# Performance work log

Measured on AMD Instinct MI355X. Metric: run time of the kernel, lower is better.

Reference implementation:

```python
import jax, jax.numpy as jnp
import numpy as np

# dims: N batch, L seq, H heads, d projection_dim, P position_dimension
N, Lq, Lk, H, d, P = 2, 1024, 1024, 8, 64, 1
D = H * d


def _kernel(x):
    # _log_exp_kernel: positive feature map log(1+exp(x)) (softplus)
    return jax.nn.softplus(x)


def setup_inputs() -> dict:
    key = jax.random.key(0)
    ks = jax.random.split(key, 8)
    sc = 1.0 / np.sqrt(D).astype(np.float32)
    return {
        "query": jax.random.normal(ks[0], (N, Lq, D), jnp.float32),
        "key_seq": jax.random.normal(ks[1], (N, Lk, D), jnp.float32),
        "Wq": jax.random.normal(ks[2], (D, D), jnp.float32) * sc,
        "Wk": jax.random.normal(ks[3], (D, D), jnp.float32) * sc,
        "Wv": jax.random.normal(ks[4], (D, D), jnp.float32) * sc,
        "position_coeffs": jax.random.uniform(ks[5], (H, d), jnp.float32, 0.5, 1.5),
        "position_weight": jax.random.normal(ks[6], (H, d, P), jnp.float32) * 1e-3,
        "position_bias": jax.random.normal(ks[7], (H, d), jnp.float32) * 1e-2,
    }


def reference(query, key_seq, Wq, Wk, Wv, position_coeffs, position_weight, position_bias):
    # torch Linear (no bias): y = x @ W.T
    q = _kernel(jnp.einsum('nld,ed->nle', query, Wq).reshape(N, Lq, H, d))
    k = _kernel(jnp.einsum('nld,ed->nle', key_seq, Wk).reshape(N, Lk, H, d))
    v = jnp.einsum('nld,ed->nle', key_seq, Wv).reshape(N, Lk, H, d)
    # (N, H, L, d)
    q = jnp.transpose(q, (0, 2, 1, 3))
    k = jnp.transpose(k, (0, 2, 1, 3))
    v = jnp.transpose(v, (0, 2, 1, 3))

    # default positions: arange, query_offset = 0
    qpos = jnp.broadcast_to(jnp.arange(Lq, dtype=jnp.float32).reshape(1, Lq, 1), (N, Lq, P))
    kpos = jnp.broadcast_to(jnp.arange(Lk, dtype=jnp.float32).reshape(1, Lk, 1), (N, Lk, P))
    pq = jnp.einsum('nlp,hkp->nhlk', qpos, position_weight) + position_bias[None, :, None, :]
    pk = jnp.einsum('nlp,hkp->nhlk', kpos, position_weight)

    coeff = position_coeffs[None, :, None, :]  # (1, H, 1, d)

    def part(f, values):
        # causal (mask_future) linear attention via inclusive cumsum over keys
        Qf = q * f(pq) * coeff           # (N, H, Lq, d)
        Kf = k * f(pk)                   # (N, H, Lk, d)
        S = jnp.cumsum(jnp.einsum('nhkd,nhke->nhkde', Kf, values), axis=2)
        return jnp.einsum('nhqd,nhqde->nhqe', Qf, S)

    num = part(jnp.cos, v) + part(jnp.sin, v)           # (N, H, Lq, d)
    unit = jnp.ones((N, H, Lk, 1), jnp.float32)
    den = part(jnp.cos, unit) + part(jnp.sin, unit)     # (N, H, Lq, 1)
    attn = num / den
    return jnp.transpose(attn, (0, 2, 1, 3)).reshape(N, Lq, D)
```

## Files before the change

### kernel.cpp

```cpp
#include <hip/hip_runtime.h>
#include <cmath>

#define NB    2
#define LSEQ  1024
#define NH    8
#define HD    64
#define DD    512
#define FDIM  128
#define EV    65
#define SEP   80
#define CHUNK 64
#define NC    16
#define NBH   16

typedef short short8 __attribute__((ext_vector_type(8)));
typedef float floatx4 __attribute__((ext_vector_type(4)));

__device__ __forceinline__ float softplusf(float x) {
  return fmaxf(x, 0.0f) + log1pf(expf(-fabsf(x)));
}

__device__ __forceinline__ unsigned short f2bf(float f) {
  unsigned u = __float_as_uint(f);
  u += 0x7fffu + ((u >> 16) & 1u);
  return (unsigned short)(u >> 16);
}

__device__ __forceinline__ short8 cvt8(float4 a, float4 b) {
  short8 r;
  r[0] = (short)f2bf(a.x); r[1] = (short)f2bf(a.y);
  r[2] = (short)f2bf(a.z); r[3] = (short)f2bf(a.w);
  r[4] = (short)f2bf(b.x); r[5] = (short)f2bf(b.y);
  r[6] = (short)f2bf(b.z); r[7] = (short)f2bf(b.w);
  return r;
}

__global__ __launch_bounds__(256) void k_proj(
    const float* __restrict__ Xq, const float* __restrict__ Xkv,
    const float* __restrict__ Wq, const float* __restrict__ Wk,
    const float* __restrict__ Wv, const float* __restrict__ pw,
    const float* __restrict__ pb, const float* __restrict__ pc,
    float* __restrict__ Qf, float* __restrict__ Kf, float* __restrict__ Vx)
{
  __shared__ short Al[64][72];
  __shared__ short Bl[64][72];
  const int b = blockIdx.x;
  int m0, e0, pmode;
  const float *X, *W;
  if (b < 256) {
    m0 = (b >> 3) << 6; e0 = (b & 7) << 6;
    X = Xq; W = Wq + (size_t)e0 * DD; pmode = 0;
  } else {
    const int bb = b - 256;
    m0 = (bb >> 4) << 6;
    const int nt = bb & 15;
    e0 = (nt & 7) << 6;
    X = Xkv;
    if (nt < 8) { W = Wk + (size_t)e0 * DD; pmode = 1; }
    else        { W = Wv + (size_t)e0 * DD; pmode = 2; }
  }
  const int tid  = threadIdx.x;
  const int r    = tid >> 2;
  const int ko   = (tid & 3) << 4;
  const int wave = tid >> 6, lane = tid & 63;
  const int quad = lane >> 4, lm = lane & 15;
  const float* Ag = X + (size_t)(m0 + r) * DD + ko;
  const float* Bg = W + (size_t)r * DD + ko;
  float4 a[4], bb4[4];
#pragma unroll
  for (int u = 0; u < 4; ++u) {
    a[u]   = *(const float4*)(Ag + (u << 2));
    bb4[u] = *(const float4*)(Bg + (u << 2));
  }
  floatx4 acc[4] = {};
  for (int k0 = 0; k0 < DD; k0 += 64) {
    __syncthreads();
    *(short8*)&Al[r][ko]     = cvt8(a[0], a[1]);
    *(short8*)&Al[r][ko + 8] = cvt8(a[2], a[3]);
    *(short8*)&Bl[r][ko]     = cvt8(bb4[0], bb4[1]);
    *(short8*)&Bl[r][ko + 8] = cvt8(bb4[2], bb4[3]);
    __syncthreads();
    if (k0 + 64 < DD) {
#pragma unroll
      for (int u = 0; u < 4; ++u) {
        a[u]   = *(const float4*)(Ag + k0 + 64 + (u << 2));
        bb4[u] = *(const float4*)(Bg + k0 + 64 + (u << 2));
      }
    }
#pragma unroll
    for (int ks = 0; ks < 2; ++ks) {
      const short8 af = *(const short8*)&Al[(wave << 4) + lm][(quad << 3) + (ks << 5)];
#pragma unroll
      for (int t = 0; t < 4; ++t) {
        const short8 bf = *(const short8*)&Bl[(t << 4) + lm][(quad << 3) + (ks << 5)];
        acc[t] = __builtin_amdgcn_mfma_f32_16x16x32_bf16(af, bf, acc[t], 0, 0, 0);
      }
    }
  }
#pragma unroll
  for (int t = 0; t < 4; ++t) {
    const int e = e0 + (t << 4) + lm;
    const int h = e >> 6, jj = e & 63;
    if (pmode == 2) {
#pragma unroll
      for (int rg = 0; rg < 4; ++rg) {
        const int m = m0 + (wave << 4) + (quad << 2) + rg;
        const int n = m >> 10, l = m & 1023;
        Vx[((size_t)(n * NH + h) * LSEQ + l) * HD + jj] = acc[t][rg];
      }
    } else {
      const float pwv = pw[e];
      const float pbv = (pmode == 0) ? pb[e] : 0.0f;
      const float pcv = (pmode == 0) ? pc[e] : 1.0f;
      float* base = (pmode == 0) ? Qf : Kf;
#pragma unroll
      for (int rg = 0; rg < 4; ++rg) {
        const int m = m0 + (wave << 4) + (quad << 2) + rg;
        const int n = m >> 10, l = m & 1023;
        const float v = softplusf(acc[t][rg]) * pcv;
        const float ang = fmaf((float)l, pwv, pbv);
        const float sn = __sinf(ang), cs = __cosf(ang);
        float* dst = &base[((size_t)(n * NH + h) * LSEQ + l) * FDIM + jj];
        dst[0]  = v * cs;
        dst[64] = v * sn;
      }
    }
  }
}

__global__ __launch_bounds__(256) void k_chunk_sums(
    const float* __restrict__ Kf, const float* __restrict__ Vx,
    float* __restrict__ S)
{
  const int blk = blockIdx.x;
  const int bh  = blk >> 5;
  const int c   = (blk >> 1) & (NC - 1);
  const int fh  = blk & 1;
  const int f0  = fh << 6;
  const int t0  = c * CHUNK;
  const int tid  = threadIdx.x;
  const int wave = tid >> 6, lane = tid & 63;
  const int quad = lane >> 4, lm = lane & 15;

  __shared__ short KT[64][72];
  __shared__ short VT[80][72];

  for (int i = tid; i < 64 * 16; i += 256) {
    const int t = i & 63, f4 = (i >> 6) << 2;
    const float4 k4 = *(const float4*)&Kf[((size_t)bh * LSEQ + t0 + t) * FDIM + f0 + f4];
    KT[f4 + 0][t] = (short)f2bf(k4.x);
    KT[f4 + 1][t] = (short)f2bf(k4.y);
    KT[f4 + 2][t] = (short)f2bf(k4.z);
    KT[f4 + 3][t] = (short)f2bf(k4.w);
  }
  for (int i = tid; i < 64 * 16; i += 256) {
    const int t = i & 63, e4 = (i >> 6) << 2;
    const float4 v4 = *(const float4*)&Vx[((size_t)bh * LSEQ + t0 + t) * HD + e4];
    VT[e4 + 0][t] = (short)f2bf(v4.x);
    VT[e4 + 1][t] = (short)f2bf(v4.y);
    VT[e4 + 2][t] = (short)f2bf(v4.z);
    VT[e4 + 3][t] = (short)f2bf(v4.w);
  }
  if (tid < CHUNK) VT[64][tid] = (short)0x3F80;
  __syncthreads();

  short8 aK[2];
#pragma unroll
  for (int ks = 0; ks < 2; ++ks)
    aK[ks] = *(const short8*)&KT[(wave << 4) + lm][(quad << 3) + (ks << 5)];
  floatx4 acc[5] = {};
#pragma unroll
  for (int nt = 0; nt < 5; ++nt)
#pragma unroll
    for (int ks = 0; ks < 2; ++ks) {
      const short8 bf = *(const short8*)&VT[(nt << 4) + lm][(quad << 3) + (ks << 5)];
      acc[nt] = __builtin_amdgcn_mfma_f32_16x16x32_bf16(aK[ks], bf, acc[nt], 0, 0, 0);
    }

  float* Sb = &S[(size_t)(bh * NC + c) * SEP * FDIM];
#pragma unroll
  for (int nt = 0; nt < 4; ++nt)
#pragma unroll
    for (int rg = 0; rg < 4; ++rg) {
      const int f = f0 + (wave << 4) + (quad << 2) + rg;
      Sb[((nt << 4) + lm) * FDIM + f] = acc[nt][rg];
    }
  if (lm == 0) {
#pragma unroll
    for (int rg = 0; rg < 4; ++rg) {
      const int f = f0 + (wave << 4) + (quad << 2) + rg;
      Sb[64 * FDIM + f] = acc[4][rg];
    }
  }
}

__global__ __launch_bounds__(256) void k_chunk_out(
    const float* __restrict__ Qf, const float* __restrict__ Kf,
    const float* __restrict__ Vx, const float* __restrict__ S,
    float* __restrict__ Out)
{
  const int c  = blockIdx.x & (NC - 1);
  const int bh = blockIdx.x >> 4;
  const int n  = bh >> 3, h = bh & 7;
  const int t0 = c * CHUNK;
  const int tid  = threadIdx.x;
  const int wave = tid >> 6, lane = tid & 63;
  const int quad = lane >> 4, lm = lane & 15;

  __shared__ short QL[64][128];
  __shared__ short KL[64][128];
  __shared__ short ScL[64][72];
  __shared__ short PT[80][136];
  __shared__ short VT[80][72];
  __shared__ float DenL[64];

  const float* Qg = &Qf[((size_t)bh * LSEQ + t0) * FDIM];
  const float* Kg = &Kf[((size_t)bh * LSEQ + t0) * FDIM];
  {
    const int f8 = (tid & 15) << 3;
#pragma unroll
    for (int rr = 0; rr < 64; rr += 16) {
      const int r = rr + (tid >> 4);
      const float4 a0 = *(const float4*)&Qg[r * FDIM + f8];
      const float4 a1 = *(const float4*)&Qg[r * FDIM + f8 + 4];
      *(short8*)&QL[r][f8] = cvt8(a0, a1);
      const float4 b0 = *(const float4*)&Kg[r * FDIM + f8];
      const float4 b1 = *(const float4*)&Kg[r * FDIM + f8 + 4];
      *(short8*)&KL[r][f8] = cvt8(b0, b1);
    }
  }
  {
    const float* Sg = &S[(size_t)(bh * NC) * SEP * FDIM];
    for (int i0 = tid; i0 < SEP * FDIM; i0 += 256 * 8) {
      float s[8] = {};
      for (int cc = 0; cc < c; ++cc) {
        const float* p = Sg + (size_t)cc * SEP * FDIM + i0;
#pragma unroll
        for (int u = 0; u < 8; ++u) s[u] += p[u * 256];
      }
#pragma unroll
      for (int u = 0; u < 8; ++u) {
        const int i = i0 + u * 256;
        PT[i >> 7][i & 127] = (short)f2bf(s[u]);
      }
    }
  }
  {
    const float* Vg = &Vx[((size_t)bh * LSEQ + t0) * HD];
    for (int i = tid; i < CHUNK * (HD / 4); i += 256) {
      const int t = i >> 4, e4 = (i & 15) << 2;
      const float4 v4 = *(const float4*)&Vg[t * HD + e4];
      VT[e4 + 0][t] = (short)f2bf(v4.x);
      VT[e4 + 1][t] = (short)f2bf(v4.y);
      VT[e4 + 2][t] = (short)f2bf(v4.z);
      VT[e4 + 3][t] = (short)f2bf(v4.w);
    }
    if (tid < CHUNK) VT[64][tid] = (short)0x3F80;
  }
  __syncthreads();

  short8 aQ[4];
#pragma unroll
  for (int ks = 0; ks < 4; ++ks)
    aQ[ks] = *(const short8*)&QL[(wave << 4) + lm][(quad << 3) + (ks << 5)];

  floatx4 accS[4] = {};
#pragma unroll
  for (int nt = 0; nt < 4; ++nt)
#pragma unroll
    for (int ks = 0; ks < 4; ++ks) {
      const short8 b = *(const short8*)&KL[(nt << 4) + lm][(quad << 3) + (ks << 5)];
      accS[nt] = __builtin_amdgcn_mfma_f32_16x16x32_bf16(aQ[ks], b, accS[nt], 0, 0, 0);
    }
#pragma unroll
  for (int nt = 0; nt < 4; ++nt)
#pragma unroll
    for (int rg = 0; rg < 4; ++rg) {
      const int m = (wave << 4) + (quad << 2) + rg;
      const int t = (nt << 4) + lm;
      ScL[m][t] = (short)((t <= m) ? f2bf(accS[nt][rg]) : 0);
    }

  floatx4 accN[5] = {};
#pragma unroll
  for (int nt = 0; nt < 5; ++nt)
#pragma unroll
    for (int ks = 0; ks < 4; ++ks) {
      const short8 b = *(const short8*)&PT[(nt << 4) + lm][(quad << 3) + (ks << 5)];
      accN[nt] = __builtin_amdgcn_mfma_f32_16x16x32_bf16(aQ[ks], b, accN[nt], 0, 0, 0);
    }

  short8 aS[2];
#pragma unroll
  for (int ks = 0; ks < 2; ++ks)
    aS[ks] = *(const short8*)&ScL[(wave << 4) + lm][(quad << 3) + (ks << 5)];
  floatx4 accV[5] = {};
#pragma unroll
  for (int nt = 0; nt < 5; ++nt)
#pragma unroll
    for (int ks = 0; ks < 2; ++ks) {
      const short8 b = *(const short8*)&VT[(nt << 4) + lm][(quad << 3) + (ks << 5)];
      accV[nt] = __builtin_amdgcn_mfma_f32_16x16x32_bf16(aS[ks], b, accV[nt], 0, 0, 0);
    }

  if (lm == 0) {
#pragma unroll
    for (int rg = 0; rg < 4; ++rg)
      DenL[(wave << 4) + (quad << 2) + rg] = accN[4][rg] + accV[4][rg];
  }

#pragma unroll
  for (int rg = 0; rg < 4; ++rg) {
    const int m = (wave << 4) + (quad << 2) + rg;
    const float rden = 1.0f / DenL[m];
    const int l = t0 + m;
#pragma unroll
    for (int nt = 0; nt < 4; ++nt) {
      const float val = (accN[nt][rg] + accV[nt][rg]) * rden;
      Out[((size_t)(n * LSEQ + l)) * DD + h * HD + (nt << 4) + lm] = val;
    }
  }
}

extern "C" void kernel_launch(void* const* d_in, const int* in_sizes, int n_in,
                              void* d_out, int out_size, void* d_ws, size_t ws_size,
                              hipStream_t stream) {
  (void)in_sizes; (void)n_in; (void)out_size; (void)ws_size;
  const float* query  = (const float*)d_in[0];
  const float* keyseq = (const float*)d_in[1];
  const float* Wq     = (const float*)d_in[2];
  const float* Wk     = (const float*)d_in[3];
  const float* Wv     = (const float*)d_in[4];
  const float* pc     = (const float*)d_in[5];
  const float* pw     = (const float*)d_in[6];
  const float* pb     = (const float*)d_in[7];
  float* out = (float*)d_out;

  float* ws = (float*)d_ws;
  float* Qf = ws;
  float* Kf = Qf + (size_t)NBH * LSEQ * FDIM;
  float* Vx = Kf + (size_t)NBH * LSEQ * FDIM;
  float* S  = Vx + (size_t)NBH * LSEQ * HD;

  k_proj      <<<768,          256, 0, stream>>>(query, keyseq, Wq, Wk, Wv, pw, pb, pc, Qf, Kf, Vx);
  k_chunk_sums<<<NBH * NC * 2, 256, 0, stream>>>(Kf, Vx, S);
  k_chunk_out <<<NBH * NC,     256, 0, stream>>>(Qf, Kf, Vx, S, out);
}
```

Measured before the change: 129.9 us.

## Add dedicated exclusive-scan kernel for chunk state prefix sums

Previously each output block recomputed the prefix sum of all earlier chunk states itself, so total work and reads grew quadratically with the chunk count. A new k_scan kernel computes an exclusive prefix over the 16 chunks once per head and element, and writes bf16 results to a workspace buffer. k_chunk_out then loads its precomputed prefix state with vector copies. The cost is one extra kernel launch and an extra workspace write and read.

Result: faster. 115.7 us (-10.9%).

```diff
diff --git a/kernel.cpp b/kernel.cpp
--- a/kernel.cpp
+++ b/kernel.cpp
@@ -15,15 +15,16 @@
 
 typedef short short8 __attribute__((ext_vector_type(8)));
 typedef float floatx4 __attribute__((ext_vector_type(4)));
+typedef unsigned short ushort;
 
 __device__ __forceinline__ float softplusf(float x) {
   return fmaxf(x, 0.0f) + log1pf(expf(-fabsf(x)));
 }
 
-__device__ __forceinline__ unsigned short f2bf(float f) {
+__device__ __forceinline__ ushort f2bf(float f) {
   unsigned u = __float_as_uint(f);
   u += 0x7fffu + ((u >> 16) & 1u);
-  return (unsigned short)(u >> 16);
+  return (ushort)(u >> 16);
 }
 
 __device__ __forceinline__ short8 cvt8(float4 a, float4 b) {
@@ -194,9 +195,33 @@
   }
 }
 
+__global__ __launch_bounds__(256) void k_scan(
+    const float* __restrict__ S, ushort* __restrict__ PTb)
+{
+  const int bh = blockIdx.x / 13;
+  const int eg = blockIdx.x % 13;
+  const size_t cs = (size_t)SEP * FDIM;
+  const float* Sg = S + (size_t)bh * NC * cs;
+  ushort* Pg = PTb + (size_t)bh * NC * cs;
+  for (int i = threadIdx.x; i < 5 * FDIM; i += 256) {
+    const int e = eg * 5 + (i >> 7);
+    const int f = i & 127;
+    const int off = e * FDIM + f;
+    float v[NC];
+#pragma unroll
+    for (int c = 0; c < NC; ++c) v[c] = Sg[(size_t)c * cs + off];
+    float s = 0.0f;
+#pragma unroll
+    for (int c = 0; c < NC; ++c) {
+      Pg[(size_t)c * cs + off] = f2bf(s);
+      s += v[c];
+    }
+  }
+}
+
 __global__ __launch_bounds__(256) void k_chunk_out(
     const float* __restrict__ Qf, const float* __restrict__ Kf,
-    const float* __restrict__ Vx, const float* __restrict__ S,
+    const float* __restrict__ Vx, const ushort* __restrict__ PTb,
     float* __restrict__ Out)
 {
   const int c  = blockIdx.x & (NC - 1);
@@ -230,19 +255,10 @@
     }
   }
   {
-    const float* Sg = &S[(size_t)(bh * NC) * SEP * FDIM];
-    for (int i0 = tid; i0 < SEP * FDIM; i0 += 256 * 8) {
-      float s[8] = {};
-      for (int cc = 0; cc < c; ++cc) {
-        const float* p = Sg + (size_t)cc * SEP * FDIM + i0;
-#pragma unroll
-        for (int u = 0; u < 8; ++u) s[u] += p[u * 256];
-      }
-#pragma unroll
-      for (int u = 0; u < 8; ++u) {
-        const int i = i0 + u * 256;
-        PT[i >> 7][i & 127] = (short)f2bf(s[u]);
-      }
+    const ushort* Pg = &PTb[(size_t)(bh * NC + c) * SEP * FDIM];
+    for (int i = tid; i < 65 * 16; i += 256) {
+      const int e = i >> 4, f8 = (i & 15) << 3;
+      *(short8*)&PT[e][f8] = *(const short8*)&Pg[e * FDIM + f8];
     }
   }
   {
@@ -337,12 +353,14 @@
   float* out = (float*)d_out;
 
   float* ws = (float*)d_ws;
-  float* Qf = ws;
-  float* Kf = Qf + (size_t)NBH * LSEQ * FDIM;
-  float* Vx = Kf + (size_t)NBH * LSEQ * FDIM;
-  float* S  = Vx + (size_t)NBH * LSEQ * HD;
+  float*  Qf  = ws;
+  float*  Kf  = Qf + (size_t)NBH * LSEQ * FDIM;
+  float*  Vx  = Kf + (size_t)NBH * LSEQ * FDIM;
+  float*  S   = Vx + (size_t)NBH * LSEQ * HD;
+  ushort* PTb = (ushort*)(S + (size_t)NBH * NC * SEP * FDIM);
 
   k_proj      <<<768,          256, 0, stream>>>(query, keyseq, Wq, Wk, Wv, pw, pb, pc, Qf, Kf, Vx);
   k_chunk_sums<<<NBH * NC * 2, 256, 0, stream>>>(Kf, Vx, S);
-  k_chunk_out <<<NBH * NC,     256, 0, stream>>>(Qf, Kf, Vx, S, out);
-}
+  k_scan      <<<NBH * 13,     256, 0, stream>>>(S, PTb);
+  k_chunk_out <<<NBH * NC,     256, 0, stream>>>(Qf, Kf, Vx, PTb, out);
+}
```
